# Kernel optimization log

Hardware: AMD Instinct MI355X
Metric: run time of the kernel (lower is better)

The kernel has to match this reference:

```python
import jax, jax.numpy as jnp
import numpy as np

T = 8192
INPUT = 1024
TRACE = 64
CTX = 16
OUT = 1024
EPS = 1e-5  # equinox LayerNorm default


def _linear(key, out_f, in_f):
    k1, k2 = jax.random.split(key)
    lim = 1.0 / np.sqrt(in_f)
    w = jax.random.uniform(k1, (out_f, in_f), minval=-lim, maxval=lim, dtype=jnp.float32)
    b = jax.random.uniform(k2, (out_f,), minval=-lim, maxval=lim, dtype=jnp.float32)
    return w, b


def setup_inputs() -> dict:
    key = jax.random.key(0)
    ks = jax.random.split(key, 8)
    x = jax.random.normal(ks[0], (T, INPUT), dtype=jnp.float32)
    start = jax.random.randint(ks[1], (T,), 0, 2).astype(bool)
    next_done = jax.random.randint(ks[2], (T,), 0, 2).astype(bool)
    state_re = jnp.zeros((1, TRACE, CTX), dtype=jnp.float32)
    state_im = jnp.zeros((1, TRACE, CTX), dtype=jnp.float32)
    pre_w, pre_b = _linear(ks[3], TRACE, INPUT)
    gi_w, gi_b = _linear(ks[4], TRACE, INPUT)
    go_w, go_b = _linear(ks[5], OUT, INPUT)
    skip_w, skip_b = _linear(ks[6], OUT, INPUT)
    mix_w, mix_b = _linear(ks[7], OUT, 2 * TRACE * CTX)
    # ffa.init: deterministic decay rates a and oscillation freqs b
    ffa_a = jnp.linspace(1e-6, 0.5, TRACE, dtype=jnp.float32)
    ffa_b = (2.0 * jnp.pi / jnp.exp(jnp.linspace(jnp.log(1.0), jnp.log(1024.0), CTX))).astype(jnp.float32)
    return dict(x=x, state_re=state_re, state_im=state_im, start=start, next_done=next_done,
                pre_w=pre_w, pre_b=pre_b, gi_w=gi_w, gi_b=gi_b, go_w=go_w, go_b=go_b,
                skip_w=skip_w, skip_b=skip_b, mix_w=mix_w, mix_b=mix_b,
                ffa_a=ffa_a, ffa_b=ffa_b)


def _ffa_apply(ffa_a, ffa_b, gated_x, state0, start):
    """Resettable complex linear recurrence: s_t = gamma * s_{t-1} + x_t, reset at episode starts.
    gamma = exp(-|a| + i b), outer over (trace, context). Parallelized with an associative scan
    over monoid elements (reset_flag, state, elapsed_steps)."""
    Tn, m = gated_x.shape
    c = ffa_b.shape[0]
    ab = jax.lax.complex(
        jnp.broadcast_to(-jnp.abs(ffa_a)[None, :, None], (1, m, c)),
        jnp.broadcast_to(ffa_b[None, None, :], (1, m, c)),
    )  # [1, m, c] complex: log-gamma per unit timestep

    xc = jnp.broadcast_to(gated_x[:, :, None].astype(jnp.complex64), (Tn, m, c))
    # prepend carried-in recurrent state: timestep 0, no reset
    x_e = jnp.concatenate([state0.astype(jnp.complex64), xc], axis=0)          # [T+1, m, c]
    s_e = jnp.concatenate([jnp.zeros((1, 1, 1), bool), start[:, None, None]], axis=0)
    i_e = jnp.concatenate([jnp.zeros((1, 1, 1), jnp.float32),
                           jnp.ones((Tn, 1, 1), jnp.float32)], axis=0)

    def op(a, b):
        s1, x1, i1 = a
        s2, x2, i2 = b
        # zero the carried state across episode boundaries
        x1 = jnp.where(s2, 0.0, x1)
        i1 = jnp.where(s2, 0.0, i1)
        g = jnp.exp(ab * i2.astype(jnp.complex64))  # decay over i2 elapsed steps
        return (jnp.logical_or(s1, s2), x1 * g + x2, i1 + i2)

    _, states, _ = jax.lax.associative_scan(op, (s_e, x_e, i_e), axis=0)
    return states[1:]  # [T, m, c] complex64


def reference(x, state_re, state_im, start, next_done,
              pre_w, pre_b, gi_w, gi_b, go_w, go_b,
              skip_w, skip_b, mix_w, mix_b, ffa_a, ffa_b):
    gate_in = jax.nn.sigmoid(x @ gi_w.T + gi_b)          # [T, trace]
    pre = x @ pre_w.T + pre_b                            # [T, trace]
    gated_x = pre * gate_in

    state0 = jax.lax.complex(state_re, state_im)         # [1, trace, ctx]
    state = _ffa_apply(ffa_a, ffa_b, gated_x, state0, start)  # [T, trace, ctx] complex

    z_in = jnp.concatenate([jnp.real(state), jnp.imag(state)], axis=-1)
    z_in = z_in.reshape(state.shape[0], -1)              # [T, 2*trace*ctx]
    z = z_in @ mix_w.T + mix_b                           # [T, out]

    gate_out = jax.nn.sigmoid(x @ go_w.T + go_b)         # [T, out]
    skip = x @ skip_w.T + skip_b                         # [T, out]

    zg = z * gate_out
    mu = zg.mean(-1, keepdims=True)
    var = ((zg - mu) ** 2).mean(-1, keepdims=True)
    ln = (zg - mu) / jnp.sqrt(var + EPS)                 # LayerNorm, no affine

    out = ln + skip * (1.0 - gate_out)
    final_state = state[-1:]
    return out, final_state


if __name__ == "__main__":
    inp = setup_inputs()
    out, fs = jax.jit(reference)(**inp)
    print(out.shape, out.dtype, fs.shape, fs.dtype)
```

## Files before the change

kernel.cpp:

```cpp
#include <hip/hip_runtime.h>
#include <math.h>

#define T_DIM 8192
#define IN_DIM 1024
#define TRACE 64
#define CTX 16
#define OUT_DIM 1024
#define KMIX 2048

typedef __attribute__((ext_vector_type(8))) short bf16x8;
typedef __attribute__((ext_vector_type(4))) float f32x4;

__device__ __forceinline__ unsigned short f2bf(float f) {
    unsigned int u = __float_as_uint(f);
    u = (u + 0x7FFFu + ((u >> 16) & 1u)) >> 16;
    return (unsigned short)u;
}
__device__ __forceinline__ float bf2f(unsigned short b) {
    return __uint_as_float(((unsigned int)b) << 16);
}

__device__ __forceinline__ void gl2lds16(const void* g, void* l) {
    __builtin_amdgcn_global_load_lds(
        (const __attribute__((address_space(1))) unsigned int*)g,
        (__attribute__((address_space(3))) unsigned int*)l,
        16, 0, 0);
}


__global__ void k0_start(const void* __restrict__ startp, unsigned char* __restrict__ mask)
{
    __shared__ int nonbool;
    int tid = threadIdx.x;
    if (tid == 0) nonbool = 0;
    __syncthreads();
    const unsigned int* w = (const unsigned int*)startp;
    unsigned int a = w[tid];
    unsigned int b = w[tid + 1024];
    if (a > 1u || b > 1u) nonbool = 1;
    __syncthreads();
    if (nonbool) {
        const unsigned char* s8 = (const unsigned char*)startp;
        for (int i = tid; i < T_DIM; i += 1024) mask[i] = (unsigned char)(s8[i] != 0);
    } else {
        const int* s32 = (const int*)startp;
        for (int i = tid; i < T_DIM; i += 1024) mask[i] = (unsigned char)(s32[i] != 0);
    }
}

__global__ __launch_bounds__(256) void c0_conv(const float* __restrict__ x,
        const float* __restrict__ gw, const float* __restrict__ sw, const float* __restrict__ mw,
        const float* __restrict__ pw, const float* __restrict__ giw,
        unsigned short* __restrict__ xb, unsigned short* __restrict__ gob,
        unsigned short* __restrict__ skb, unsigned short* __restrict__ mixb,
        unsigned short* __restrict__ pwb, unsigned short* __restrict__ gwb)
{
    const size_t QX = 2097152, QG = 262144, QS = 262144, QM = 524288, QP = 16384, QI = 16384;
    const size_t total = QX + QG + QS + QM + QP + QI;
    for (size_t q = (size_t)blockIdx.x * blockDim.x + threadIdx.x; q < total;
         q += (size_t)gridDim.x * blockDim.x) {
        const float* src; unsigned short* dst; size_t i;
        if (q < QX)                  { src = x;   dst = xb;   i = q; }
        else if (q < QX+QG)          { src = gw;  dst = gob;  i = q - QX; }
        else if (q < QX+QG+QS)       { src = sw;  dst = skb;  i = q - QX - QG; }
        else if (q < QX+QG+QS+QM)    { src = mw;  dst = mixb; i = q - QX - QG - QS; }
        else if (q < QX+QG+QS+QM+QP) { src = pw;  dst = pwb;  i = q - QX - QG - QS - QM; }
        else                         { src = giw; dst = gwb;  i = q - QX - QG - QS - QM - QP; }
        float4 v = *(const float4*)(src + i * 4);
        ushort4 o;
        o.x = f2bf(v.x); o.y = f2bf(v.y); o.z = f2bf(v.z); o.w = f2bf(v.w);
        *(ushort4*)(dst + i * 4) = o;
    }
}

__global__ __launch_bounds__(256) void k1_mfma(const unsigned short* __restrict__ xb,
        const unsigned short* __restrict__ pwb, const unsigned short* __restrict__ gwb,
        const float* __restrict__ pre_b, const float* __restrict__ gi_b,
        float* __restrict__ gxT)
{
    __shared__ __align__(16) unsigned short As[4096];
    __shared__ __align__(16) unsigned short Bs[4096];
    __shared__ float sgE[64][133];

    const int tid = threadIdx.x;
    const int t0 = blockIdx.x * 128;
    const int lane = tid & 63, w = tid >> 6;
    const int wm = w >> 1, wn = w & 1;
    const int quad = lane >> 4, l16 = lane & 15;
    const int r = tid >> 2, c = (tid & 3) * 8;

    const unsigned short* gA0 = xb  + (size_t)(t0 + r)      * IN_DIM + c;
    const unsigned short* gA1 = xb  + (size_t)(t0 + 64 + r) * IN_DIM + c;
    const unsigned short* gB0 = pwb + (size_t)r * IN_DIM + c;
    const unsigned short* gB1 = gwb + (size_t)r * IN_DIM + c;
    unsigned short* lA0 = As + tid * 8;
    unsigned short* lA1 = As + 2048 + tid * 8;
    unsigned short* lB0 = Bs + tid * 8;
    unsigned short* lB1 = Bs + 2048 + tid * 8;

    f32x4 acc[4][4];
    const f32x4 zero4 = {0.f, 0.f, 0.f, 0.f};
    #pragma unroll
    for (int mi = 0; mi < 4; mi++)
        #pragma unroll
        for (int ni = 0; ni < 4; ni++) acc[mi][ni] = zero4;

    for (int k0 = 0; k0 < IN_DIM; k0 += 32) {
        __syncthreads();
        gl2lds16(gA0 + k0, lA0);
        gl2lds16(gA1 + k0, lA1);
        gl2lds16(gB0 + k0, lB0);
        gl2lds16(gB1 + k0, lB1);
        asm volatile("s_waitcnt vmcnt(0)" ::: "memory");
        __syncthreads();
        bf16x8 af[4], bf[4];
        #pragma unroll
        for (int mi = 0; mi < 4; mi++)
            af[mi] = *(const bf16x8*)&As[(wm * 64 + mi * 16 + l16) * 32 + quad * 8];
        #pragma unroll
        for (int ni = 0; ni < 4; ni++)
            bf[ni] = *(const bf16x8*)&Bs[(wn * 64 + ni * 16 + l16) * 32 + quad * 8];
        #pragma unroll
        for (int mi = 0; mi < 4; mi++)
            #pragma unroll
            for (int ni = 0; ni < 4; ni++)
                acc[mi][ni] = __builtin_amdgcn_mfma_f32_16x16x32_bf16(af[mi], bf[ni], acc[mi][ni], 0, 0, 0);
    }

    if (wn == 1) {
        #pragma unroll
        for (int mi = 0; mi < 4; mi++)
            #pragma unroll
            for (int ni = 0; ni < 4; ni++) {
                int mg = ni * 16 + l16;
                float gb = gi_b[mg];
                #pragma unroll
                for (int rr = 0; rr < 4; rr++) {
                    int tl = wm * 64 + mi * 16 + quad * 4 + rr;
                    sgE[mg][tl] = 1.f / (1.f + expf(-(acc[mi][ni][rr] + gb)));
                }
            }
    }
    __syncthreads();
    if (wn == 0) {
        #pragma unroll
        for (int mi = 0; mi < 4; mi++)
            #pragma unroll
            for (int ni = 0; ni < 4; ni++) {
                int mp = ni * 16 + l16;
                float pb = pre_b[mp];
                #pragma unroll
                for (int rr = 0; rr < 4; rr++) {
                    int tl = wm * 64 + mi * 16 + quad * 4 + rr;
                    gxT[(size_t)mp * T_DIM + t0 + tl] = (acc[mi][ni][rr] + pb) * sgE[mp][tl];
                }
            }
    }
}

__global__ __launch_bounds__(128) void k2_scan(const float* __restrict__ gxT,
        const unsigned char* __restrict__ mask8,
        const float* __restrict__ state_re, const float* __restrict__ state_im,
        const float* __restrict__ ffa_a, const float* __restrict__ ffa_b,
        unsigned short* __restrict__ zinTb, float* __restrict__ fstate)
{
    const int m = blockIdx.x >> 4;
    const int c = blockIdx.x & 15;
    const int j = threadIdx.x;
    __shared__ float Br[128], Bi[128], Er[128], Ei[128];
    __shared__ unsigned char Rf[128];

    const float am = -fabsf(ffa_a[m]);
    const float bc = ffa_b[c];
    const float er = expf(am);
    const float gr = er * cosf(bc);
    const float gi = er * sinf(bc);

    const float* gx = gxT + (size_t)m * T_DIM;
    const int t0 = j * 64;

    unsigned long long rmask = 0ull;
    float sre = 0.f, sim = 0.f;
    bool r = false;
    #pragma unroll 8
    for (int i = 0; i < 64; i++) {
        int t = t0 + i;
        if (mask8[t]) { rmask |= 1ull << i; sre = 0.f; sim = 0.f; r = true; }
        else { float tr_ = sre * gr - sim * gi; sim = sre * gi + sim * gr; sre = tr_; }
        sre += gx[t];
    }
    Br[j] = sre; Bi[j] = sim; Rf[j] = r ? 1 : 0;
    __syncthreads();
    if (j == 0) {
        float e64  = expf(64.f * am);
        float g64r = e64 * cosf(64.f * bc);
        float g64i = e64 * sinf(64.f * bc);
        float pr = state_re[m * CTX + c], pi = state_im[m * CTX + c];
        for (int q = 0; q < 128; q++) {
            Er[q] = pr; Ei[q] = pi;
            if (Rf[q]) { pr = Br[q]; pi = Bi[q]; }
            else {
                float nr = pr * g64r - pi * g64i + Br[q];
                pi       = pr * g64i + pi * g64r + Bi[q];
                pr = nr;
            }
        }
    }
    __syncthreads();
    sre = Er[j]; sim = Ei[j];
    unsigned int ore[32], oim[32];
    #pragma unroll
    for (int i = 0; i < 64; i++) {
        int t = t0 + i;
        if (rmask & (1ull << i)) { sre = 0.f; sim = 0.f; }
        else { float tr_ = sre * gr - sim * gi; sim = sre * gi + sim * gr; sre = tr_; }
        sre += gx[t];
        unsigned short hr = f2bf(sre), hi_ = f2bf(sim);
        if (i & 1) { ore[i >> 1] |= ((unsigned int)hr) << 16; oim[i >> 1] |= ((unsigned int)hi_) << 16; }
        else       { ore[i >> 1]  = hr;                        oim[i >> 1]  = hi_; }
    }
    unsigned short* zreb = zinTb + (size_t)(m * 32 + c)      * T_DIM;
    unsigned short* zimb = zinTb + (size_t)(m * 32 + 16 + c) * T_DIM;
    uint4* pre4 = (uint4*)(zreb + t0);
    uint4* pim4 = (uint4*)(zimb + t0);
    #pragma unroll
    for (int q = 0; q < 8; q++) pre4[q] = *(uint4*)&ore[q * 4];
    #pragma unroll
    for (int q = 0; q < 8; q++) pim4[q] = *(uint4*)&oim[q * 4];

    if (j == 127) {
        int p = m * CTX + c;
        fstate[p]        = sre;
        fstate[1024 + p] = sim;
    }
}

__global__ __launch_bounds__(256) void t3_tr(const unsigned short* __restrict__ zinTb,
                                             unsigned short* __restrict__ zinb)
{
    __shared__ unsigned short S[64][72];
    const int k0 = blockIdx.x * 64, t0 = blockIdx.y * 64;
    const int tid = threadIdx.x;
    {
        int kr = tid >> 3, tc = (tid & 7) * 8;
        #pragma unroll
        for (int p = 0; p < 2; p++) {
            int k = kr + p * 32;
            ushort4 a = *(const ushort4*)&zinTb[(size_t)(k0 + k) * T_DIM + t0 + tc];
            ushort4 b = *(const ushort4*)&zinTb[(size_t)(k0 + k) * T_DIM + t0 + tc + 4];
            *(ushort4*)&S[k][tc]     = a;
            *(ushort4*)&S[k][tc + 4] = b;
        }
    }
    __syncthreads();
    {
        int tr = tid >> 3, kc = (tid & 7) * 8;
        #pragma unroll
        for (int p = 0; p < 2; p++) {
            int t = tr + p * 32;
            ushort4 o1, o2;
            o1.x = S[kc+0][t]; o1.y = S[kc+1][t]; o1.z = S[kc+2][t]; o1.w = S[kc+3][t];
            o2.x = S[kc+4][t]; o2.y = S[kc+5][t]; o2.z = S[kc+6][t]; o2.w = S[kc+7][t];
            *(ushort4*)&zinb[(size_t)(t0 + t) * KMIX + k0 + kc]     = o1;
            *(ushort4*)&zinb[(size_t)(t0 + t) * KMIX + k0 + kc + 4] = o2;
        }
    }
}

__global__ __launch_bounds__(256, 2) void gA_gemm(
        const unsigned short* __restrict__ xb,   const unsigned short* __restrict__ zinb,
        const unsigned short* __restrict__ gob,  const unsigned short* __restrict__ skb,
        const unsigned short* __restrict__ mixb,
        const float* __restrict__ go_b, const float* __restrict__ skip_b, const float* __restrict__ mix_b,
        unsigned short* __restrict__ zg, unsigned short* __restrict__ sk2)
{
    __shared__ __align__(16) unsigned short As[4096];
    __shared__ __align__(16) unsigned short Bs[4096];
    __shared__ __align__(16) unsigned short Cs[4096];
    const int tid = threadIdx.x;
    const int b = blockIdx.x;
    const int xcd = b & 7, q = b >> 3;
    const int t0 = (xcd * 8 + (q >> 3)) * 128;
    const int n0 = (q & 7) * 128;

    const int lane = tid & 63, w = tid >> 6;
    const int wm = w >> 1, wn = w & 1;
    const int quad = lane >> 4, l16 = lane & 15;
    const int r = tid >> 2, c = (tid & 3) * 8;

    unsigned short* lA0 = As + tid * 8;
    unsigned short* lA1 = As + 2048 + tid * 8;
    unsigned short* lB0 = Bs + tid * 8;
    unsigned short* lB1 = Bs + 2048 + tid * 8;
    unsigned short* lC0 = Cs + tid * 8;
    unsigned short* lC1 = Cs + 2048 + tid * 8;

    f32x4 accg[4][4], acck[4][4];
    const f32x4 zero4 = {0.f, 0.f, 0.f, 0.f};
    #pragma unroll
    for (int mi = 0; mi < 4; mi++)
        #pragma unroll
        for (int ni = 0; ni < 4; ni++) { accg[mi][ni] = zero4; acck[mi][ni] = zero4; }

    {
        const unsigned short* gA0 = xb  + (size_t)(t0 + r)      * IN_DIM + c;
        const unsigned short* gA1 = xb  + (size_t)(t0 + 64 + r) * IN_DIM + c;
        const unsigned short* gB0 = gob + (size_t)(n0 + r)      * IN_DIM + c;
        const unsigned short* gB1 = gob + (size_t)(n0 + 64 + r) * IN_DIM + c;
        const unsigned short* gC0 = skb + (size_t)(n0 + r)      * IN_DIM + c;
        const unsigned short* gC1 = skb + (size_t)(n0 + 64 + r) * IN_DIM + c;
        for (int k0 = 0; k0 < IN_DIM; k0 += 32) {
            __syncthreads();
            gl2lds16(gA0 + k0, lA0);
            gl2lds16(gA1 + k0, lA1);
            gl2lds16(gB0 + k0, lB0);
            gl2lds16(gB1 + k0, lB1);
            gl2lds16(gC0 + k0, lC0);
            gl2lds16(gC1 + k0, lC1);
            asm volatile("s_waitcnt vmcnt(0)" ::: "memory");
            __syncthreads();
            bf16x8 af[4], bg[4], bk[4];
            #pragma unroll
            for (int mi = 0; mi < 4; mi++)
                af[mi] = *(const bf16x8*)&As[(wm * 64 + mi * 16 + l16) * 32 + quad * 8];
            #pragma unroll
            for (int ni = 0; ni < 4; ni++) {
                bg[ni] = *(const bf16x8*)&Bs[(wn * 64 + ni * 16 + l16) * 32 + quad * 8];
                bk[ni] = *(const bf16x8*)&Cs[(wn * 64 + ni * 16 + l16) * 32 + quad * 8];
            }
            #pragma unroll
            for (int mi = 0; mi < 4; mi++)
                #pragma unroll
                for (int ni = 0; ni < 4; ni++) {
                    accg[mi][ni] = __builtin_amdgcn_mfma_f32_16x16x32_bf16(af[mi], bg[ni], accg[mi][ni], 0, 0, 0);
                    acck[mi][ni] = __builtin_amdgcn_mfma_f32_16x16x32_bf16(af[mi], bk[ni], acck[mi][ni], 0, 0, 0);
                }
        }
    }

    unsigned int sigp[32];
    #pragma unroll
    for (int mi = 0; mi < 4; mi++)
        #pragma unroll
        for (int ni = 0; ni < 4; ni++) {
            int n = n0 + wn * 64 + ni * 16 + l16;
            float gb = go_b[n];
            float sb_ = skip_b[n];
            #pragma unroll
            for (int r2 = 0; r2 < 2; r2++) {
                float s0 = 1.f / (1.f + expf(-(accg[mi][ni][r2 * 2]     + gb)));
                float s1 = 1.f / (1.f + expf(-(accg[mi][ni][r2 * 2 + 1] + gb)));
                sigp[(mi * 4 + ni) * 2 + r2] =
                    (unsigned int)f2bf(s0) | ((unsigned int)f2bf(s1) << 16);
                int t = t0 + wm * 64 + mi * 16 + quad * 4 + r2 * 2;
                sk2[(size_t)t * OUT_DIM + n]       = f2bf((acck[mi][ni][r2*2]   + sb_) * (1.f - s0));
                sk2[(size_t)(t+1) * OUT_DIM + n]   = f2bf((acck[mi][ni][r2*2+1] + sb_) * (1.f - s1));
            }
        }

    #pragma unroll
    for (int mi = 0; mi < 4; mi++)
        #pragma unroll
        for (int ni = 0; ni < 4; ni++) accg[mi][ni] = zero4;
    {
        const unsigned short* gA0 = zinb + (size_t)(t0 + r)      * KMIX + c;
        const unsigned short* gA1 = zinb + (size_t)(t0 + 64 + r) * KMIX + c;
        const unsigned short* gB0 = mixb + (size_t)(n0 + r)      * KMIX + c;
        const unsigned short* gB1 = mixb + (size_t)(n0 + 64 + r) * KMIX + c;
        for (int k0 = 0; k0 < KMIX; k0 += 32) {
            __syncthreads();
            gl2lds16(gA0 + k0, lA0);
            gl2lds16(gA1 + k0, lA1);
            gl2lds16(gB0 + k0, lB0);
            gl2lds16(gB1 + k0, lB1);
            asm volatile("s_waitcnt vmcnt(0)" ::: "memory");
            __syncthreads();
            bf16x8 af[4], bf[4];
            #pragma unroll
            for (int mi = 0; mi < 4; mi++)
                af[mi] = *(const bf16x8*)&As[(wm * 64 + mi * 16 + l16) * 32 + quad * 8];
            #pragma unroll
            for (int ni = 0; ni < 4; ni++)
                bf[ni] = *(const bf16x8*)&Bs[(wn * 64 + ni * 16 + l16) * 32 + quad * 8];
            #pragma unroll
            for (int mi = 0; mi < 4; mi++)
                #pragma unroll
                for (int ni = 0; ni < 4; ni++)
                    accg[mi][ni] = __builtin_amdgcn_mfma_f32_16x16x32_bf16(af[mi], bf[ni], accg[mi][ni], 0, 0, 0);
        }
    }

    #pragma unroll
    for (int mi = 0; mi < 4; mi++)
        #pragma unroll
        for (int ni = 0; ni < 4; ni++) {
            int n = n0 + wn * 64 + ni * 16 + l16;
            float mb_ = mix_b[n];
            #pragma unroll
            for (int rr = 0; rr < 4; rr++) {
                unsigned int u = sigp[(mi * 4 + ni) * 2 + (rr >> 1)];
                float sig = bf2f((unsigned short)((rr & 1) ? (u >> 16) : (u & 0xffff)));
                float v = (accg[mi][ni][rr] + mb_) * sig;
                int t = t0 + wm * 64 + mi * 16 + quad * 4 + rr;
                zg[(size_t)t * OUT_DIM + n] = f2bf(v);
            }
        }
}

__global__ __launch_bounds__(256) void g3_ln(const unsigned short* __restrict__ zg,
        const unsigned short* __restrict__ sk2, float* __restrict__ out)
{
    __shared__ float sb[4], qb[4];
    __shared__ float mu_s, rstd_s;
    const int t = blockIdx.x;
    const int tid = threadIdx.x;
    ushort4 zu = *(const ushort4*)&zg [(size_t)t * OUT_DIM + tid * 4];
    ushort4 su = *(const ushort4*)&sk2[(size_t)t * OUT_DIM + tid * 4];
    float z0 = bf2f(zu.x), z1 = bf2f(zu.y), z2 = bf2f(zu.z), z3 = bf2f(zu.w);
    float s0 = bf2f(su.x), s1 = bf2f(su.y), s2 = bf2f(su.z), s3 = bf2f(su.w);
    float s = z0 + z1 + z2 + z3;
    float q = z0*z0 + z1*z1 + z2*z2 + z3*z3;
    #pragma unroll
    for (int off = 32; off > 0; off >>= 1) {
        s += __shfl_down(s, off, 64);
        q += __shfl_down(q, off, 64);
    }
    int wid = tid >> 6;
    if ((tid & 63) == 0) { sb[wid] = s; qb[wid] = q; }
    __syncthreads();
    if (tid == 0) {
        float S = sb[0] + sb[1] + sb[2] + sb[3];
        float Q = qb[0] + qb[1] + qb[2] + qb[3];
        float mu = S * (1.f / 1024.f);
        float var = Q * (1.f / 1024.f) - mu * mu;
        mu_s = mu; rstd_s = rsqrtf(var + 1e-5f);
    }
    __syncthreads();
    float mu = mu_s, rs = rstd_s;
    float4 o;
    o.x = (z0 - mu) * rs + s0;
    o.y = (z1 - mu) * rs + s1;
    o.z = (z2 - mu) * rs + s2;
    o.w = (z3 - mu) * rs + s3;
    *(float4*)&out[(size_t)t * OUT_DIM + tid * 4] = o;
}

__global__ void g4_final(const float* __restrict__ fstate, float* __restrict__ out, int out_size)
{
    int i = blockIdx.x * blockDim.x + threadIdx.x;
    if (i >= 2048) return;
    long long base = (long long)T_DIM * OUT_DIM;
    if (base + i < (long long)out_size) out[base + i] = fstate[i];
}

extern "C" void kernel_launch(void* const* d_in, const int* in_sizes, int n_in,
                              void* d_out, int out_size, void* d_ws, size_t ws_size,
                              hipStream_t stream) {
    const float* x        = (const float*)d_in[0];
    const float* state_re = (const float*)d_in[1];
    const float* state_im = (const float*)d_in[2];
    const void*  startp   = d_in[3];
    const float* pre_w    = (const float*)d_in[5];
    const float* pre_b    = (const float*)d_in[6];
    const float* gi_w     = (const float*)d_in[7];
    const float* gi_b     = (const float*)d_in[8];
    const float* go_w     = (const float*)d_in[9];
    const float* go_b     = (const float*)d_in[10];
    const float* skip_w   = (const float*)d_in[11];
    const float* skip_b   = (const float*)d_in[12];
    const float* mix_w    = (const float*)d_in[13];
    const float* mix_b    = (const float*)d_in[14];
    const float* ffa_a    = (const float*)d_in[15];
    const float* ffa_b    = (const float*)d_in[16];

    float* ws = (float*)d_ws;
    float*          gxT    = ws;
    unsigned short* zinTb  = (unsigned short*)(ws + 524288);
    unsigned short* zinb   = (unsigned short*)(ws + 8912896);
    unsigned short* xb     = (unsigned short*)(ws + 17301504);
    unsigned short* gob    = (unsigned short*)(ws + 21495808);
    unsigned short* skb    = (unsigned short*)(ws + 22020096);
    unsigned short* mixb   = (unsigned short*)(ws + 22544384);
    unsigned short* zg     = (unsigned short*)(ws + 23592960);
    unsigned short* sk2    = (unsigned short*)(ws + 27787264);
    float*          fstate = ws + 31981568;
    unsigned char*  mask   = (unsigned char*)(ws + 31983616);
    unsigned short* pwb    = zg;
    unsigned short* gwb    = zg + 65536;
    float* out = (float*)d_out;

    hipLaunchKernelGGL(k0_start, dim3(1),       dim3(1024), 0, stream, startp, mask);
    hipLaunchKernelGGL(c0_conv,  dim3(1536),    dim3(256),  0, stream, x, go_w, skip_w, mix_w, pre_w, gi_w,
                                                             xb, gob, skb, mixb, pwb, gwb);
    hipLaunchKernelGGL(k1_mfma,  dim3(64),      dim3(256),  0, stream, xb, pwb, gwb, pre_b, gi_b, gxT);
    hipLaunchKernelGGL(k2_scan,  dim3(1024),    dim3(128),  0, stream, gxT, mask, state_re, state_im, ffa_a, ffa_b, zinTb, fstate);
    hipLaunchKernelGGL(t3_tr,    dim3(32, 128), dim3(256),  0, stream, zinTb, zinb);
    hipLaunchKernelGGL(gA_gemm,  dim3(512),     dim3(256),  0, stream, xb, zinb, gob, skb, mixb, go_b, skip_b, mix_b, zg, sk2);
    hipLaunchKernelGGL(g3_ln,    dim3(8192),    dim3(256),  0, stream, zg, sk2, out);
    hipLaunchKernelGGL(g4_final, dim3(8),       dim3(256),  0, stream, fstate, out, out_size);
}
```

Measured before the change: 320.3 us.

## Retile k1 for more blocks, coalesce scan stores, use 32x32 MFMA in main GEMM

k1 now uses 32-row tiles and launches 256 blocks instead of 64, so more CUs get work, and it writes gxT as float4. The scan kernel stages its bf16 outputs through shared memory so global stores are contiguous across threads instead of strided per thread. The fused gate/skip/mix GEMM switches from 16x16x32 to 32x32x16 bf16 MFMA with f32x16 accumulators, which cuts LDS fragment loads per FLOP. The trade-offs are extra shared memory and barriers in the scan kernel, and register pressure from the larger accumulators.

After: 305.0 us. 1.05x faster.

```diff
diff --git a/kernel.cpp b/kernel.cpp
--- a/kernel.cpp
+++ b/kernel.cpp
@@ -10,6 +10,7 @@
 
 typedef __attribute__((ext_vector_type(8))) short bf16x8;
 typedef __attribute__((ext_vector_type(4))) float f32x4;
+typedef __attribute__((ext_vector_type(16))) float f32x16;
 
 __device__ __forceinline__ unsigned short f2bf(float f) {
     unsigned int u = __float_as_uint(f);
@@ -78,82 +79,75 @@
         const float* __restrict__ pre_b, const float* __restrict__ gi_b,
         float* __restrict__ gxT)
 {
-    __shared__ __align__(16) unsigned short As[4096];
+    __shared__ __align__(16) unsigned short As[1024];
     __shared__ __align__(16) unsigned short Bs[4096];
-    __shared__ float sgE[64][133];
+    __shared__ float sgE[64][33];
 
     const int tid = threadIdx.x;
-    const int t0 = blockIdx.x * 128;
+    const int t0 = blockIdx.x * 32;
     const int lane = tid & 63, w = tid >> 6;
-    const int wm = w >> 1, wn = w & 1;
     const int quad = lane >> 4, l16 = lane & 15;
-    const int r = tid >> 2, c = (tid & 3) * 8;
-
-    const unsigned short* gA0 = xb  + (size_t)(t0 + r)      * IN_DIM + c;
-    const unsigned short* gA1 = xb  + (size_t)(t0 + 64 + r) * IN_DIM + c;
-    const unsigned short* gB0 = pwb + (size_t)r * IN_DIM + c;
-    const unsigned short* gB1 = gwb + (size_t)r * IN_DIM + c;
-    unsigned short* lA0 = As + tid * 8;
-    unsigned short* lA1 = As + 2048 + tid * 8;
-    unsigned short* lB0 = Bs + tid * 8;
-    unsigned short* lB1 = Bs + 2048 + tid * 8;
-
-    f32x4 acc[4][4];
+    const int r = tid >> 2, c8 = (tid & 3) * 8;
+
+    f32x4 acc[2][2];
     const f32x4 zero4 = {0.f, 0.f, 0.f, 0.f};
     #pragma unroll
-    for (int mi = 0; mi < 4; mi++)
-        #pragma unroll
-        for (int ni = 0; ni < 4; ni++) acc[mi][ni] = zero4;
+    for (int mi = 0; mi < 2; mi++)
+        #pragma unroll
+        for (int ni = 0; ni < 2; ni++) acc[mi][ni] = zero4;
 
     for (int k0 = 0; k0 < IN_DIM; k0 += 32) {
         __syncthreads();
-        gl2lds16(gA0 + k0, lA0);
-        gl2lds16(gA1 + k0, lA1);
-        gl2lds16(gB0 + k0, lB0);
-        gl2lds16(gB1 + k0, lB1);
+        if (tid < 128)
+            gl2lds16(xb + (size_t)(t0 + (tid >> 2)) * IN_DIM + k0 + (tid & 3) * 8, As + tid * 8);
+        gl2lds16(pwb + (size_t)r * IN_DIM + k0 + c8, Bs + tid * 8);
+        gl2lds16(gwb + (size_t)r * IN_DIM + k0 + c8, Bs + 2048 + tid * 8);
         asm volatile("s_waitcnt vmcnt(0)" ::: "memory");
         __syncthreads();
-        bf16x8 af[4], bf[4];
-        #pragma unroll
-        for (int mi = 0; mi < 4; mi++)
-            af[mi] = *(const bf16x8*)&As[(wm * 64 + mi * 16 + l16) * 32 + quad * 8];
-        #pragma unroll
-        for (int ni = 0; ni < 4; ni++)
-            bf[ni] = *(const bf16x8*)&Bs[(wn * 64 + ni * 16 + l16) * 32 + quad * 8];
-        #pragma unroll
-        for (int mi = 0; mi < 4; mi++)
-            #pragma unroll
-            for (int ni = 0; ni < 4; ni++)
+        bf16x8 af[2], bf[2];
+        #pragma unroll
+        for (int mi = 0; mi < 2; mi++)
+            af[mi] = *(const bf16x8*)&As[(mi * 16 + l16) * 32 + quad * 8];
+        #pragma unroll
+        for (int ni = 0; ni < 2; ni++)
+            bf[ni] = *(const bf16x8*)&Bs[(w * 32 + ni * 16 + l16) * 32 + quad * 8];
+        #pragma unroll
+        for (int mi = 0; mi < 2; mi++)
+            #pragma unroll
+            for (int ni = 0; ni < 2; ni++)
                 acc[mi][ni] = __builtin_amdgcn_mfma_f32_16x16x32_bf16(af[mi], bf[ni], acc[mi][ni], 0, 0, 0);
     }
 
-    if (wn == 1) {
-        #pragma unroll
-        for (int mi = 0; mi < 4; mi++)
-            #pragma unroll
-            for (int ni = 0; ni < 4; ni++) {
-                int mg = ni * 16 + l16;
+    if (w >= 2) {
+        #pragma unroll
+        for (int mi = 0; mi < 2; mi++)
+            #pragma unroll
+            for (int ni = 0; ni < 2; ni++) {
+                int mg = (w - 2) * 32 + ni * 16 + l16;
                 float gb = gi_b[mg];
                 #pragma unroll
                 for (int rr = 0; rr < 4; rr++) {
-                    int tl = wm * 64 + mi * 16 + quad * 4 + rr;
+                    int tl = mi * 16 + quad * 4 + rr;
                     sgE[mg][tl] = 1.f / (1.f + expf(-(acc[mi][ni][rr] + gb)));
                 }
             }
     }
     __syncthreads();
-    if (wn == 0) {
-        #pragma unroll
-        for (int mi = 0; mi < 4; mi++)
-            #pragma unroll
-            for (int ni = 0; ni < 4; ni++) {
-                int mp = ni * 16 + l16;
+    if (w < 2) {
+        #pragma unroll
+        for (int mi = 0; mi < 2; mi++)
+            #pragma unroll
+            for (int ni = 0; ni < 2; ni++) {
+                int mp = w * 32 + ni * 16 + l16;
                 float pb = pre_b[mp];
+                float4 o;
+                float* po = &o.x;
                 #pragma unroll
                 for (int rr = 0; rr < 4; rr++) {
-                    int tl = wm * 64 + mi * 16 + quad * 4 + rr;
-                    gxT[(size_t)mp * T_DIM + t0 + tl] = (acc[mi][ni][rr] + pb) * sgE[mp][tl];
+                    int tl = mi * 16 + quad * 4 + rr;
+                    po[rr] = (acc[mi][ni][rr] + pb) * sgE[mp][tl];
                 }
+                *(float4*)&gxT[(size_t)mp * T_DIM + t0 + mi * 16 + quad * 4] = o;
             }
     }
 }
@@ -169,6 +163,7 @@
     const int j = threadIdx.x;
     __shared__ float Br[128], Bi[128], Er[128], Ei[128];
     __shared__ unsigned char Rf[128];
+    __shared__ unsigned int SB[128 * 33];
 
     const float am = -fabsf(ffa_a[m]);
     const float bc = ffa_b[c];
@@ -219,19 +214,35 @@
         if (i & 1) { ore[i >> 1] |= ((unsigned int)hr) << 16; oim[i >> 1] |= ((unsigned int)hi_) << 16; }
         else       { ore[i >> 1]  = hr;                        oim[i >> 1]  = hi_; }
     }
-    unsigned short* zreb = zinTb + (size_t)(m * 32 + c)      * T_DIM;
-    unsigned short* zimb = zinTb + (size_t)(m * 32 + 16 + c) * T_DIM;
-    uint4* pre4 = (uint4*)(zreb + t0);
-    uint4* pim4 = (uint4*)(zimb + t0);
-    #pragma unroll
-    for (int q = 0; q < 8; q++) pre4[q] = *(uint4*)&ore[q * 4];
-    #pragma unroll
-    for (int q = 0; q < 8; q++) pim4[q] = *(uint4*)&oim[q * 4];
-
     if (j == 127) {
         int p = m * CTX + c;
         fstate[p]        = sre;
         fstate[1024 + p] = sim;
+    }
+
+    unsigned short* zreb = zinTb + (size_t)(m * 32 + c)      * T_DIM;
+    unsigned short* zimb = zinTb + (size_t)(m * 32 + 16 + c) * T_DIM;
+
+    #pragma unroll
+    for (int q = 0; q < 32; q++) SB[j * 33 + q] = ore[q];
+    __syncthreads();
+    #pragma unroll
+    for (int it = 0; it < 8; it++) {
+        int g = (it * 128 + j) * 4;
+        int jj = g >> 5, qq = g & 31;
+        uint4 v = *(uint4*)&SB[jj * 33 + qq];
+        *(uint4*)(zreb + g * 2) = v;
+    }
+    __syncthreads();
+    #pragma unroll
+    for (int q = 0; q < 32; q++) SB[j * 33 + q] = oim[q];
+    __syncthreads();
+    #pragma unroll
+    for (int it = 0; it < 8; it++) {
+        int g = (it * 128 + j) * 4;
+        int jj = g >> 5, qq = g & 31;
+        uint4 v = *(uint4*)&SB[jj * 33 + qq];
+        *(uint4*)(zimb + g * 2) = v;
     }
 }
 
@@ -285,8 +296,8 @@
 
     const int lane = tid & 63, w = tid >> 6;
     const int wm = w >> 1, wn = w & 1;
-    const int quad = lane >> 4, l16 = lane & 15;
-    const int r = tid >> 2, c = (tid & 3) * 8;
+    const int l31 = lane & 31, h = lane >> 5;
+    const int r = tid >> 2, c8 = (tid & 3) * 8;
 
     unsigned short* lA0 = As + tid * 8;
     unsigned short* lA1 = As + 2048 + tid * 8;
@@ -295,20 +306,21 @@
     unsigned short* lC0 = Cs + tid * 8;
     unsigned short* lC1 = Cs + 2048 + tid * 8;
 
-    f32x4 accg[4][4], acck[4][4];
-    const f32x4 zero4 = {0.f, 0.f, 0.f, 0.f};
-    #pragma unroll
-    for (int mi = 0; mi < 4; mi++)
-        #pragma unroll
-        for (int ni = 0; ni < 4; ni++) { accg[mi][ni] = zero4; acck[mi][ni] = zero4; }
+    f32x16 accg[2][2], acck[2][2];
+    #pragma unroll
+    for (int mi = 0; mi < 2; mi++)
+        #pragma unroll
+        for (int ni = 0; ni < 2; ni++)
+            #pragma unroll
+            for (int e = 0; e < 16; e++) { accg[mi][ni][e] = 0.f; acck[mi][ni][e] = 0.f; }
 
     {
-        const unsigned short* gA0 = xb  + (size_t)(t0 + r)      * IN_DIM + c;
-        const unsigned short* gA1 = xb  + (size_t)(t0 + 64 + r) * IN_DIM + c;
-        const unsigned short* gB0 = gob + (size_t)(n0 + r)      * IN_DIM + c;
-        const unsigned short* gB1 = gob + (size_t)(n0 + 64 + r) * IN_DIM + c;
-        const unsigned short* gC0 = skb + (size_t)(n0 + r)      * IN_DIM + c;
-        const unsigned short* gC1 = skb + (size_t)(n0 + 64 + r) * IN_DIM + c;
+        const unsigned short* gA0 = xb  + (size_t)(t0 + r)      * IN_DIM + c8;
+        const unsigned short* gA1 = xb  + (size_t)(t0 + 64 + r) * IN_DIM + c8;
+        const unsigned short* gB0 = gob + (size_t)(n0 + r)      * IN_DIM + c8;
+        const unsigned short* gB1 = gob + (size_t)(n0 + 64 + r) * IN_DIM + c8;
+        const unsigned short* gC0 = skb + (size_t)(n0 + r)      * IN_DIM + c8;
+        const unsigned short* gC1 = skb + (size_t)(n0 + 64 + r) * IN_DIM + c8;
         for (int k0 = 0; k0 < IN_DIM; k0 += 32) {
             __syncthreads();
             gl2lds16(gA0 + k0, lA0);
@@ -319,54 +331,60 @@
             gl2lds16(gC1 + k0, lC1);
             asm volatile("s_waitcnt vmcnt(0)" ::: "memory");
             __syncthreads();
-            bf16x8 af[4], bg[4], bk[4];
-            #pragma unroll
-            for (int mi = 0; mi < 4; mi++)
-                af[mi] = *(const bf16x8*)&As[(wm * 64 + mi * 16 + l16) * 32 + quad * 8];
-            #pragma unroll
-            for (int ni = 0; ni < 4; ni++) {
-                bg[ni] = *(const bf16x8*)&Bs[(wn * 64 + ni * 16 + l16) * 32 + quad * 8];
-                bk[ni] = *(const bf16x8*)&Cs[(wn * 64 + ni * 16 + l16) * 32 + quad * 8];
-            }
-            #pragma unroll
-            for (int mi = 0; mi < 4; mi++)
-                #pragma unroll
-                for (int ni = 0; ni < 4; ni++) {
-                    accg[mi][ni] = __builtin_amdgcn_mfma_f32_16x16x32_bf16(af[mi], bg[ni], accg[mi][ni], 0, 0, 0);
-                    acck[mi][ni] = __builtin_amdgcn_mfma_f32_16x16x32_bf16(af[mi], bk[ni], acck[mi][ni], 0, 0, 0);
+            #pragma unroll
+            for (int kh = 0; kh < 2; kh++) {
+                bf16x8 af[2], bg[2], bk[2];
+                #pragma unroll
+                for (int mi = 0; mi < 2; mi++)
+                    af[mi] = *(const bf16x8*)&As[(wm * 64 + mi * 32 + l31) * 32 + kh * 16 + h * 8];
+                #pragma unroll
+                for (int ni = 0; ni < 2; ni++) {
+                    bg[ni] = *(const bf16x8*)&Bs[(wn * 64 + ni * 32 + l31) * 32 + kh * 16 + h * 8];
+                    bk[ni] = *(const bf16x8*)&Cs[(wn * 64 + ni * 32 + l31) * 32 + kh * 16 + h * 8];
                 }
+                #pragma unroll
+                for (int mi = 0; mi < 2; mi++)
+                    #pragma unroll
+                    for (int ni = 0; ni < 2; ni++) {
+                        accg[mi][ni] = __builtin_amdgcn_mfma_f32_32x32x16_bf16(af[mi], bg[ni], accg[mi][ni], 0, 0, 0);
+                        acck[mi][ni] = __builtin_amdgcn_mfma_f32_32x32x16_bf16(af[mi], bk[ni], acck[mi][ni], 0, 0, 0);
+                    }
+            }
         }
     }
 
     unsigned int sigp[32];
     #pragma unroll
-    for (int mi = 0; mi < 4; mi++)
-        #pragma unroll
-        for (int ni = 0; ni < 4; ni++) {
-            int n = n0 + wn * 64 + ni * 16 + l16;
+    for (int mi = 0; mi < 2; mi++)
+        #pragma unroll
+        for (int ni = 0; ni < 2; ni++) {
+            int n = n0 + wn * 64 + ni * 32 + l31;
             float gb = go_b[n];
             float sb_ = skip_b[n];
             #pragma unroll
-            for (int r2 = 0; r2 < 2; r2++) {
-                float s0 = 1.f / (1.f + expf(-(accg[mi][ni][r2 * 2]     + gb)));
-                float s1 = 1.f / (1.f + expf(-(accg[mi][ni][r2 * 2 + 1] + gb)));
-                sigp[(mi * 4 + ni) * 2 + r2] =
-                    (unsigned int)f2bf(s0) | ((unsigned int)f2bf(s1) << 16);
-                int t = t0 + wm * 64 + mi * 16 + quad * 4 + r2 * 2;
-                sk2[(size_t)t * OUT_DIM + n]       = f2bf((acck[mi][ni][r2*2]   + sb_) * (1.f - s0));
-                sk2[(size_t)(t+1) * OUT_DIM + n]   = f2bf((acck[mi][ni][r2*2+1] + sb_) * (1.f - s1));
-            }
-        }
-
-    #pragma unroll
-    for (int mi = 0; mi < 4; mi++)
-        #pragma unroll
-        for (int ni = 0; ni < 4; ni++) accg[mi][ni] = zero4;
+            for (int reg = 0; reg < 16; reg++) {
+                int row = (reg & 3) + 8 * (reg >> 2) + 4 * h;
+                int t = t0 + wm * 64 + mi * 32 + row;
+                float s = 1.f / (1.f + expf(-(accg[mi][ni][reg] + gb)));
+                sk2[(size_t)t * OUT_DIM + n] = f2bf((acck[mi][ni][reg] + sb_) * (1.f - s));
+                unsigned int pk = (unsigned int)f2bf(s);
+                int idx = (mi * 2 + ni) * 8 + (reg >> 1);
+                if (reg & 1) sigp[idx] |= pk << 16;
+                else         sigp[idx]  = pk;
+            }
+        }
+
+    #pragma unroll
+    for (int mi = 0; mi < 2; mi++)
+        #pragma unroll
+        for (int ni = 0; ni < 2; ni++)
+            #pragma unroll
+            for (int e = 0; e < 16; e++) accg[mi][ni][e] = 0.f;
     {
-        const unsigned short* gA0 = zinb + (size_t)(t0 + r)      * KMIX + c;
-        const unsigned short* gA1 = zinb + (size_t)(t0 + 64 + r) * KMIX + c;
-        const unsigned short* gB0 = mixb + (size_t)(n0 + r)      * KMIX + c;
-        const unsigned short* gB1 = mixb + (size_t)(n0 + 64 + r) * KMIX + c;
+        const unsigned short* gA0 = zinb + (size_t)(t0 + r)      * KMIX + c8;
+        const unsigned short* gA1 = zinb + (size_t)(t0 + 64 + r) * KMIX + c8;
+        const unsigned short* gB0 = mixb + (size_t)(n0 + r)      * KMIX + c8;
+        const unsigned short* gB1 = mixb + (size_t)(n0 + 64 + r) * KMIX + c8;
         for (int k0 = 0; k0 < KMIX; k0 += 32) {
             __syncthreads();
             gl2lds16(gA0 + k0, lA0);
@@ -375,34 +393,37 @@
             gl2lds16(gB1 + k0, lB1);
             asm volatile("s_waitcnt vmcnt(0)" ::: "memory");
             __syncthreads();
-            bf16x8 af[4], bf[4];
-            #pragma unroll
-            for (int mi = 0; mi < 4; mi++)
-                af[mi] = *(const bf16x8*)&As[(wm * 64 + mi * 16 + l16) * 32 + quad * 8];
-            #pragma unroll
-            for (int ni = 0; ni < 4; ni++)
-                bf[ni] = *(const bf16x8*)&Bs[(wn * 64 + ni * 16 + l16) * 32 + quad * 8];
-            #pragma unroll
-            for (int mi = 0; mi < 4; mi++)
-                #pragma unroll
-                for (int ni = 0; ni < 4; ni++)
-                    accg[mi][ni] = __builtin_amdgcn_mfma_f32_16x16x32_bf16(af[mi], bf[ni], accg[mi][ni], 0, 0, 0);
-        }
-    }
-
-    #pragma unroll
-    for (int mi = 0; mi < 4; mi++)
-        #pragma unroll
-        for (int ni = 0; ni < 4; ni++) {
-            int n = n0 + wn * 64 + ni * 16 + l16;
+            #pragma unroll
+            for (int kh = 0; kh < 2; kh++) {
+                bf16x8 af[2], bf[2];
+                #pragma unroll
+                for (int mi = 0; mi < 2; mi++)
+                    af[mi] = *(const bf16x8*)&As[(wm * 64 + mi * 32 + l31) * 32 + kh * 16 + h * 8];
+                #pragma unroll
+                for (int ni = 0; ni < 2; ni++)
+                    bf[ni] = *(const bf16x8*)&Bs[(wn * 64 + ni * 32 + l31) * 32 + kh * 16 + h * 8];
+                #pragma unroll
+                for (int mi = 0; mi < 2; mi++)
+                    #pragma unroll
+                    for (int ni = 0; ni < 2; ni++)
+                        accg[mi][ni] = __builtin_amdgcn_mfma_f32_32x32x16_bf16(af[mi], bf[ni], accg[mi][ni], 0, 0, 0);
+            }
+        }
+    }
+
+    #pragma unroll
+    for (int mi = 0; mi < 2; mi++)
+        #pragma unroll
+        for (int ni = 0; ni < 2; ni++) {
+            int n = n0 + wn * 64 + ni * 32 + l31;
             float mb_ = mix_b[n];
             #pragma unroll
-            for (int rr = 0; rr < 4; rr++) {
-                unsigned int u = sigp[(mi * 4 + ni) * 2 + (rr >> 1)];
-                float sig = bf2f((unsigned short)((rr & 1) ? (u >> 16) : (u & 0xffff)));
-                float v = (accg[mi][ni][rr] + mb_) * sig;
-                int t = t0 + wm * 64 + mi * 16 + quad * 4 + rr;
-                zg[(size_t)t * OUT_DIM + n] = f2bf(v);
+            for (int reg = 0; reg < 16; reg++) {
+                int row = (reg & 3) + 8 * (reg >> 2) + 4 * h;
+                int t = t0 + wm * 64 + mi * 32 + row;
+                unsigned int u = sigp[(mi * 2 + ni) * 8 + (reg >> 1)];
+                float sig = bf2f((unsigned short)((reg & 1) ? (u >> 16) : (u & 0xffff)));
+                zg[(size_t)t * OUT_DIM + n] = f2bf((accg[mi][ni][reg] + mb_) * sig);
             }
         }
 }
@@ -492,7 +513,7 @@
     hipLaunchKernelGGL(k0_start, dim3(1),       dim3(1024), 0, stream, startp, mask);
     hipLaunchKernelGGL(c0_conv,  dim3(1536),    dim3(256),  0, stream, x, go_w, skip_w, mix_w, pre_w, gi_w,
                                                              xb, gob, skb, mixb, pwb, gwb);
-    hipLaunchKernelGGL(k1_mfma,  dim3(64),      dim3(256),  0, stream, xb, pwb, gwb, pre_b, gi_b, gxT);
+    hipLaunchKernelGGL(k1_mfma,  dim3(256),     dim3(256),  0, stream, xb, pwb, gwb, pre_b, gi_b, gxT);
     hipLaunchKernelGGL(k2_scan,  dim3(1024),    dim3(128),  0, stream, gxT, mask, state_re, state_im, ffa_a, ffa_b, zinTb, fstate);
     hipLaunchKernelGGL(t3_tr,    dim3(32, 128), dim3(256),  0, stream, zinTb, zinb);
     hipLaunchKernelGGL(gA_gemm,  dim3(512),     dim3(256),  0, stream, xb, zinb, gob, skb, mixb, go_b, skip_b, mix_b, zg, sk2);
```
